# Optimization experiments

Measured on AMD Instinct MI355X. Metric: run time of the kernel, lower is better.

Reference implementation:

```python
import jax, jax.numpy as jnp
import numpy as np

N_FEATURES = 128
N_QUBITS = 10
Q_DEPTH = 4
N_OUTPUTS = 1
BATCH = 32768


def _apply_1q(psi, U, w, n):
    """Apply a single-qubit gate on wire w. psi: [B, 2^n]; U: [2,2] or [B,2,2]."""
    B = psi.shape[0]
    left, right = 2 ** w, 2 ** (n - 1 - w)
    psi = psi.reshape(B, left, 2, right)
    if U.ndim == 2:
        psi = jnp.einsum('ij,bljr->blir', U, psi)
    else:
        psi = jnp.einsum('bij,bljr->blir', U, psi)
    return psi.reshape(B, -1)


def _apply_cnot(psi, c, t, n):
    """CNOT(control=c, target=t) on psi [B, 2^n] (wire 0 = most significant bit)."""
    B = psi.shape[0]
    psi = psi.reshape((B,) + (2,) * n)
    ax_c, ax_t = c + 1, t + 1
    psi0 = jnp.take(psi, 0, axis=ax_c)
    psi1 = jnp.take(psi, 1, axis=ax_c)
    ax_t2 = ax_t - 1 if ax_t > ax_c else ax_t  # target axis shifts after removing control axis
    psi1 = jnp.flip(psi1, axis=ax_t2)          # flip target bit where control == 1
    psi = jnp.stack([psi0, psi1], axis=ax_c)
    return psi.reshape(B, -1)


def _rx_batched(theta):
    """RX(theta) per sample. theta: [B] -> U: [B,2,2] complex64."""
    c = jnp.cos(0.5 * theta).astype(jnp.complex64)
    s = jnp.sin(0.5 * theta).astype(jnp.complex64)
    row0 = jnp.stack([c, -1j * s], axis=-1)
    row1 = jnp.stack([-1j * s, c], axis=-1)
    return jnp.stack([row0, row1], axis=-2)


def _rot(phi, theta, omega):
    """Pennylane Rot = RZ(omega) @ RY(theta) @ RZ(phi), scalar angles -> [2,2] complex64."""
    c = jnp.cos(0.5 * theta)
    s = jnp.sin(0.5 * theta)
    u00 = jnp.exp(-0.5j * (phi + omega)) * c
    u01 = -jnp.exp(0.5j * (phi - omega)) * s
    u10 = jnp.exp(-0.5j * (phi - omega)) * s
    u11 = jnp.exp(0.5j * (phi + omega)) * c
    return jnp.stack([jnp.stack([u00, u01]), jnp.stack([u10, u11])]).astype(jnp.complex64)


def _quantum_forward(angles, q_weights):
    """Batched statevector sim: AngleEmbedding(RX) + StronglyEntanglingLayers, PauliZ expvals."""
    B, n = angles.shape
    depth = q_weights.shape[0]
    D = 2 ** n
    psi = jnp.zeros((B, D), jnp.complex64).at[:, 0].set(1.0)
    # AngleEmbedding: RX(angles[:, w]) on each wire (per-sample angles)
    for w in range(n):
        psi = _apply_1q(psi, _rx_batched(angles[:, w]), w, n)
    # StronglyEntanglingLayers: Rot on each wire, then CNOT ring with range r
    for l in range(depth):
        for w in range(n):
            U = _rot(q_weights[l, w, 0], q_weights[l, w, 1], q_weights[l, w, 2])
            psi = _apply_1q(psi, U, w, n)
        r = (l % (n - 1)) + 1
        for w in range(n):
            psi = _apply_cnot(psi, w, (w + r) % n, n)
    probs = psi.real ** 2 + psi.imag ** 2  # [B, D]
    # <Z_i> = sum_k probs[:,k] * (+1 if bit_i(k)==0 else -1); wire 0 = MSB
    bits = (jnp.arange(D)[None, :] >> (n - 1 - jnp.arange(n))[:, None]) & 1  # [n, D]
    signs = (1.0 - 2.0 * bits).astype(jnp.float32)
    return probs @ signs.T  # [B, n]


def setup_inputs() -> dict:
    key = jax.random.key(0)
    ks = jax.random.split(key, 5)
    x = jax.random.normal(ks[0], (BATCH, N_FEATURES), jnp.float32)
    W_pre = jax.random.normal(ks[1], (N_QUBITS, N_FEATURES), jnp.float32) / np.sqrt(N_FEATURES).astype(np.float32)
    b_pre = jnp.zeros((N_QUBITS,), jnp.float32)
    q_weights = 0.01 * jax.random.normal(ks[2], (Q_DEPTH, N_QUBITS, 3), jnp.float32)
    W_post = jax.random.normal(ks[3], (N_OUTPUTS, N_QUBITS), jnp.float32) / np.sqrt(N_QUBITS).astype(np.float32)
    b_post = jnp.zeros((N_OUTPUTS,), jnp.float32)
    return {"x": x, "W_pre": W_pre, "b_pre": b_pre, "q_weights": q_weights, "W_post": W_post, "b_post": b_post}


def reference(x, W_pre, b_pre, q_weights, W_post, b_post):
    angles = jnp.tanh(x @ W_pre.T + b_pre)        # pre_net + tanh -> [B, n_qubits]
    q_out = _quantum_forward(angles, q_weights)   # PauliZ expectations [B, n_qubits]
    return jax.nn.sigmoid(q_out @ W_post.T + b_post)
```

## Files before the change

kernel.cpp:

```cpp
#include <hip/hip_runtime.h>
#include <math.h>

#define BATCH 32768

typedef unsigned int u32;

#if defined(__has_builtin)
#if __has_builtin(__builtin_amdgcn_permlane32_swap) && __has_builtin(__builtin_amdgcn_permlane16_swap)
#define USE_PERMLANE 1
#else
#define USE_PERMLANE 0
#endif
#else
#define USE_PERMLANE 0
#endif

struct GateC { unsigned prt, sel; };
struct CircuitT { GateC g[4][10]; unsigned srow[10]; };

constexpr CircuitT make_circuit() {
  CircuitT C{};
  unsigned row[10], col[10];
  for (int b = 0; b < 10; ++b) { row[b] = 1u << b; col[b] = 1u << b; }
  for (int l = 0; l < 4; ++l) {
    for (int w = 0; w < 10; ++w) {
      C.g[l][w].prt = col[9 - w];
      C.g[l][w].sel = row[9 - w];
    }
    const int r = (l % 9) + 1;
    for (int w = 0; w < 10; ++w) {
      const int c = w, t = (w + r) % 10;
      const int bc = 9 - c, bt = 9 - t;
      row[bt] ^= row[bc];
      col[bc] ^= col[bt];
    }
  }
  for (int i = 0; i < 10; ++i) C.srow[i] = row[9 - i];
  return C;
}
constexpr CircuitT CIRC = make_circuit();

template<int CTRL>
__device__ __forceinline__ u32 dppu(u32 v) {
  return (u32)__builtin_amdgcn_update_dpp((int)v, (int)v, CTRL, 0xF, 0xF, false);
}

template<int LOW>
__device__ __forceinline__ u32 dpp_low(u32 v) {
  static_assert(LOW >= 0 && LOW <= 15, "bad mask");
  if constexpr (LOW == 0) return v;
  else if constexpr (LOW == 1) return dppu<0xB1>(v);
  else if constexpr (LOW == 2) return dppu<0x4E>(v);
  else if constexpr (LOW == 3) return dppu<0x1B>(v);
  else if constexpr (LOW == 7) return dppu<0x141>(v);
  else if constexpr (LOW == 15) return dppu<0x140>(v);
  else if constexpr (LOW >= 4 && LOW <= 6) return dpp_low<LOW ^ 7>(dppu<0x141>(v));
  else return dpp_low<LOW ^ 15>(dppu<0x140>(v));
}

constexpr int dpp_ops_low(int low) {
  if (low == 0) return 0;
  if (low == 1 || low == 2 || low == 3 || low == 7 || low == 15) return 1;
  if ((low >= 4 && low <= 6) || low == 8 || (low >= 12 && low <= 14)) return 2;
  return 3;
}
constexpr int chain_cost(int M) {
#if !USE_PERMLANE
  if (M & 48) return 99;
#endif
  return ((M & 32) ? 2 : 0) + ((M & 16) ? 2 : 0) + dpp_ops_low(M & 15);
}
constexpr bool use_ds_mask(int M) { return chain_cost(M) >= 2; }

#if USE_PERMLANE
__device__ __forceinline__ u32 xor16u(u32 v, int lane) {
  auto r = __builtin_amdgcn_permlane16_swap(v, v, false, false);
  return (lane & 16) ? r[0] : r[1];
}
__device__ __forceinline__ u32 xor32u(u32 v, int lane) {
  auto r = __builtin_amdgcn_permlane32_swap(v, v, false, false);
  return (lane & 32) ? r[0] : r[1];
}
#else
__device__ __forceinline__ u32 xor16u(u32 v, int lane) { return (u32)__shfl_xor((int)v, 16, 64); }
__device__ __forceinline__ u32 xor32u(u32 v, int lane) { return (u32)__shfl_xor((int)v, 32, 64); }
#endif

template<int M>
__device__ __forceinline__ u32 lshuf(u32 v, int lane, int bpa) {
  if constexpr (use_ds_mask(M)) {
    if constexpr ((M & 32) != 0) {
      return (u32)__builtin_amdgcn_ds_bpermute(bpa, (int)v);
    } else {
      return (u32)__builtin_amdgcn_ds_swizzle((int)v, 0x1F | (M << 10));
    }
  } else {
    u32 t = v;
    if constexpr ((M & 32) != 0) t = xor32u(t, lane);
    if constexpr ((M & 16) != 0) t = xor16u(t, lane);
    if constexpr ((M & 15) != 0) t = dpp_low<M & 15>(t);
    return t;
  }
}

template<int CTRL>
__device__ __forceinline__ float dppf(float v) {
  const int i = __float_as_int(v);
  return __int_as_float(__builtin_amdgcn_update_dpp(i, i, CTRL, 0xF, 0xF, false));
}
__device__ __forceinline__ float shflx(float v, int m) { return __shfl_xor(v, m, 64); }

__device__ __forceinline__ float wave_sum(float v, int lane) {
  v += dppf<0xB1>(v);
  v += dppf<0x4E>(v);
  v += dppf<0x141>(v);
  v += dppf<0x140>(v);
#if USE_PERMLANE
  { auto r = __builtin_amdgcn_permlane16_swap(__float_as_uint(v), __float_as_uint(v), false, false);
    v = __uint_as_float(r[0]) + __uint_as_float(r[1]); }
  { auto r = __builtin_amdgcn_permlane32_swap(__float_as_uint(v), __float_as_uint(v), false, false);
    v = __uint_as_float(r[0]) + __uint_as_float(r[1]); }
#else
  v += shflx(v, 16);
  v += shflx(v, 32);
#endif
  return v;
}

__device__ __forceinline__ u32 pk_mul_h(u32 a, u32 b) {
  u32 d; asm("v_pk_mul_f16 %0, %1, %2" : "=v"(d) : "v"(a), "v"(b)); return d;
}
__device__ __forceinline__ u32 pk_fma_h(u32 a, u32 b, u32 c) {
  u32 d; asm("v_pk_fma_f16 %0, %1, %2, %3" : "=v"(d) : "v"(a), "v"(b), "v"(c)); return d;
}
__device__ __forceinline__ u32 pk_fma_hsw(u32 a, u32 b, u32 c) {
  u32 d;
  asm("v_pk_fma_f16 %0, %1, %2, %3 op_sel:[1,0,0] op_sel_hi:[0,1,1]"
      : "=v"(d) : "v"(a), "v"(b), "v"(c));
  return d;
}

__device__ __forceinline__ u32 pk2(float lo, float hi) {
  auto h = __builtin_amdgcn_cvt_pkrtz(lo, hi);
  return __builtin_bit_cast(u32, h);
}

__device__ __forceinline__ u32 updh(u32 a, u32 q, const uint4 s) {
  u32 t = pk_mul_h(a, s.x);
  t = pk_fma_hsw(a, s.y, t);
  t = pk_fma_h(q, s.z, t);
  t = pk_fma_hsw(q, s.w, t);
  return t;
}

template<int L, int W>
__device__ __forceinline__ void gate(u32 a[16], const u32* __restrict__ Ush, int lane) {
  constexpr unsigned PRT = CIRC.g[L][W].prt;
  constexpr unsigned SEL = CIRC.g[L][W].sel;
  constexpr int PLm = (int)(PRT >> 4), PRm = (int)(PRT & 15u);
  constexpr int SLm = (int)(SEL >> 4), SRm = (int)(SEL & 15u);

  int hl = 0;
  if constexpr (SLm != 0) hl = __popc(lane & SLm) & 1;

  const u32* gb = Ush + (L * 10 + W - 10) * 8;
  const uint4 cA = *(const uint4*)(gb + (hl << 2));
  uint4 cB;
  if constexpr (SRm != 0) cB = *(const uint4*)(gb + ((hl ^ 1) << 2));
  else                    cB = cA;

  int bpa = 0;
  if constexpr (use_ds_mask(PLm) && (PLm & 32) != 0) bpa = (lane ^ PLm) << 2;

  if constexpr (PLm == 0) {
    constexpr int LB = PRm & (-PRm);
#pragma unroll
    for (int t0 = 0; t0 < 16; ++t0) {
      if (t0 & LB) continue;
      const int t1 = t0 ^ PRm;
      const uint4 s0 = (__builtin_popcount((unsigned)(t0 & SRm)) & 1) ? cB : cA;
      const uint4 s1 = (__builtin_popcount((unsigned)(t1 & SRm)) & 1) ? cB : cA;
      const u32 a0 = a[t0], a1 = a[t1];
      a[t0] = updh(a0, a1, s0);
      a[t1] = updh(a1, a0, s1);
    }
  } else if constexpr (PRm == 0) {
#pragma unroll
    for (int t = 0; t < 16; ++t) {
      const u32 q = lshuf<PLm>(a[t], lane, bpa);
      const uint4 s = (__builtin_popcount((unsigned)(t & SRm)) & 1) ? cB : cA;
      a[t] = updh(a[t], q, s);
    }
  } else {
    constexpr int LB = PRm & (-PRm);
#pragma unroll
    for (int t0 = 0; t0 < 16; ++t0) {
      if (t0 & LB) continue;
      const int t1 = t0 ^ PRm;
      const u32 q0 = lshuf<PLm>(a[t1], lane, bpa);
      const u32 q1 = lshuf<PLm>(a[t0], lane, bpa);
      const uint4 s0 = (__builtin_popcount((unsigned)(t0 & SRm)) & 1) ? cB : cA;
      const uint4 s1 = (__builtin_popcount((unsigned)(t1 & SRm)) & 1) ? cB : cA;
      a[t0] = updh(a[t0], q0, s0);
      a[t1] = updh(a[t1], q1, s1);
    }
  }
}

template<int L, int W>
__device__ __forceinline__ void layer_from(u32 a[16], const u32* __restrict__ Ush, int lane) {
  if constexpr (W < 10) {
    gate<L, W>(a, Ush, lane);
    layer_from<L, W + 1>(a, Ush, lane);
  }
}

__global__ __launch_bounds__(256, 4) void qnn_kernel(
    const float* __restrict__ x, const float* __restrict__ Wpre,
    const float* __restrict__ bpre, const float* __restrict__ qw,
    const float* __restrict__ Wpost, const float* __restrict__ bpost,
    float* __restrict__ out)
{
  __shared__ __align__(16) u32 Ush[320];

  const int tid = threadIdx.x;
  if (tid < 40) {
    const float phi = qw[tid * 3 + 0];
    const float th  = qw[tid * 3 + 1];
    const float om  = qw[tid * 3 + 2];
    const float c = cosf(0.5f * th), s_ = sinf(0.5f * th);
    const float A  = c;
    const float Br = -cosf(phi) * s_, Bi = -sinf(phi) * s_;
    const float Cr =  cosf(om)  * s_, Ci =  sinf(om)  * s_;
    const float Dr =  cosf(phi + om) * c, Di = sinf(phi + om) * c;
    if (tid < 10) {
      u32* q = &Ush[240 + tid * 8];
      q[0] = __float_as_uint(A);  q[1] = __float_as_uint(Br);
      q[2] = __float_as_uint(Bi); q[3] = __float_as_uint(Cr);
      q[4] = __float_as_uint(Ci); q[5] = __float_as_uint(Dr);
      q[6] = __float_as_uint(Di); q[7] = 0u;
    } else {
      u32* p = &Ush[(tid - 10) * 8];
      p[0] = pk2(A, A);   p[1] = pk2(0.f, 0.f);
      p[2] = pk2(Br, Br); p[3] = pk2(-Bi, Bi);
      p[4] = pk2(Dr, Dr); p[5] = pk2(-Di, Di);
      p[6] = pk2(Cr, Cr); p[7] = pk2(-Ci, Ci);
    }
  }
  __syncthreads();

  const int lane = tid & 63;
  const int b = blockIdx.x * 4 + (tid >> 6);

  const float* xrow = x + (size_t)b * 128;
  const float x0 = xrow[lane];
  const float x1 = xrow[lane + 64];
  float cw[10], sw[10];
#pragma unroll
  for (int w = 0; w < 10; ++w) {
    float p = fmaf(x0, Wpre[w * 128 + lane], x1 * Wpre[w * 128 + 64 + lane]);
    p = wave_sum(p, lane);
    const float e = __expf(2.f * (p + bpre[w]));
    const float ang = 1.f - 2.f * __builtin_amdgcn_rcpf(e + 1.f);
    const float h = 0.5f * ang;
    cw[w] = __cosf(h);
    sw[w] = __sinf(h);
  }

  float u0r[10], u0i[10], u1r[10], u1i[10];
#pragma unroll
  for (int w = 0; w < 10; ++w) {
    const u32* q = &Ush[240 + w * 8];
    const float A = __uint_as_float(q[0]), Br = __uint_as_float(q[1]);
    const float Bi = __uint_as_float(q[2]), Cr = __uint_as_float(q[3]);
    const float Ci = __uint_as_float(q[4]), Dr = __uint_as_float(q[5]);
    const float Di = __uint_as_float(q[6]);
    const float ch = cw[w], sh = sw[w];
    u0r[w] = fmaf(A, ch, Bi * sh);
    u0i[w] = -Br * sh;
    u1r[w] = fmaf(Cr, ch, Di * sh);
    u1i[w] = fmaf(Ci, ch, -Dr * sh);
  }

  float Lr, Li;
  {
    const int b0 = (lane >> 5) & 1;
    Lr = b0 ? u1r[0] : u0r[0];
    Li = b0 ? u1i[0] : u0i[0];
  }
#pragma unroll
  for (int w = 1; w < 6; ++w) {
    const int bb = (lane >> (5 - w)) & 1;
    const float arv = bb ? u1r[w] : u0r[w];
    const float aiv = bb ? u1i[w] : u0i[w];
    const float nr = fmaf(Lr, arv, -Li * aiv);
    const float ni = fmaf(Lr, aiv, Li * arv);
    Lr = nr; Li = ni;
  }

  float t4r[4], t4i[4], lsr[4], lsi[4];
#pragma unroll
  for (int aa = 0; aa < 2; ++aa) {
#pragma unroll
    for (int c2 = 0; c2 < 2; ++c2) {
      const int k = (aa << 1) | c2;
      const float ar6 = aa ? u1r[6] : u0r[6], ai6 = aa ? u1i[6] : u0i[6];
      const float ar7 = c2 ? u1r[7] : u0r[7], ai7 = c2 ? u1i[7] : u0i[7];
      t4r[k] = fmaf(ar6, ar7, -ai6 * ai7);
      t4i[k] = fmaf(ar6, ai7, ai6 * ar7);
      const float ar8 = aa ? u1r[8] : u0r[8], ai8 = aa ? u1i[8] : u0i[8];
      const float ar9 = c2 ? u1r[9] : u0r[9], ai9 = c2 ? u1i[9] : u0i[9];
      const float s4r = fmaf(ar8, ar9, -ai8 * ai9);
      const float s4i = fmaf(ar8, ai9, ai8 * ar9);
      lsr[k] = fmaf(s4r, Lr, -s4i * Li);
      lsi[k] = fmaf(s4r, Li, s4i * Lr);
    }
  }

  u32 a[16];
#pragma unroll
  for (int t = 0; t < 16; ++t) {
    const int hi4 = t >> 2, lo4 = t & 3;
    const float re = fmaf(t4r[hi4], lsr[lo4], -t4i[hi4] * lsi[lo4]);
    const float im = fmaf(t4r[hi4], lsi[lo4],  t4i[hi4] * lsr[lo4]);
    a[t] = pk2(re, im);
  }

  layer_from<1, 0>(a, Ush, lane);
  layer_from<2, 0>(a, Ush, lane);
  layer_from<3, 0>(a, Ush, lane);

  float Wl[10];
#pragma unroll
  for (int i = 0; i < 10; ++i) {
    const int sl = (int)(CIRC.srow[i] >> 4);
    const int par = __popc(lane & sl) & 1;
    const float wv = Wpost[i];
    Wl[i] = par ? -wv : wv;
  }
  float G[16];
#pragma unroll
  for (int m = 0; m < 16; ++m) G[m] = 0.f;
#pragma unroll
  for (int i = 0; i < 10; ++i) G[CIRC.srow[i] & 15u] += Wl[i];
#pragma unroll
  for (int bit = 1; bit < 16; bit <<= 1) {
#pragma unroll
    for (int m = 0; m < 16; ++m) {
      if (!(m & bit)) {
        const float t = G[m];
        G[m] = t + G[m ^ bit];
        G[m ^ bit] = t - G[m ^ bit];
      }
    }
  }

  union H2U { u32 u; _Float16 h[2]; };
  float acc = 0.f;
#pragma unroll
  for (int t = 0; t < 16; ++t) {
    H2U z; z.u = a[t];
    const float rr = (float)z.h[0];
    const float ii = (float)z.h[1];
    acc = fmaf(fmaf(rr, rr, ii * ii), G[t], acc);
  }
  acc = wave_sum(acc, lane);

  if (lane == 0) {
    const float z = acc + bpost[0];
    out[b] = __builtin_amdgcn_rcpf(1.f + __expf(-z));
  }
}

extern "C" void kernel_launch(void* const* d_in, const int* in_sizes, int n_in,
                              void* d_out, int out_size, void* d_ws, size_t ws_size,
                              hipStream_t stream) {
  const float* x     = (const float*)d_in[0];
  const float* Wpre  = (const float*)d_in[1];
  const float* bpre  = (const float*)d_in[2];
  const float* qw    = (const float*)d_in[3];
  const float* Wpost = (const float*)d_in[4];
  const float* bpost = (const float*)d_in[5];
  float* out = (float*)d_out;

  (void)in_sizes; (void)n_in; (void)out_size; (void)d_ws; (void)ws_size;

  qnn_kernel<<<BATCH / 4, 256, 0, stream>>>(x, Wpre, bpre, qw, Wpost, bpost, out);
}
```

Baseline: 170.4 us.

## Precompute post-readout weight table in LDS, reorder gates, use fdot2 for probabilities

Moves the per-lane Walsh-Hadamard computation of the readout weights G into a shared 16x64 table that each block fills once. Each wave then reads its weights from LDS instead of recomputing them. Gate application order within layers 1-3 is permuted, presumably to group commuting gates and cut shuffle cost. |a|^2 is computed with a packed fp16 fdot2. The table adds LDS use and per-block setup work, and the reorder relies on those gates commuting.

Result: no change. 167.5 us (-1.7%).

```diff
diff --git a/kernel.cpp b/kernel.cpp
--- a/kernel.cpp
+++ b/kernel.cpp
@@ -11,8 +11,14 @@
 #else
 #define USE_PERMLANE 0
 #endif
+#if __has_builtin(__builtin_amdgcn_fdot2)
+#define HAS_FDOT2 1
+#else
+#define HAS_FDOT2 0
+#endif
 #else
 #define USE_PERMLANE 0
+#define HAS_FDOT2 0
 #endif
 
 struct GateC { unsigned prt, sel; };
@@ -39,6 +45,13 @@
   return C;
 }
 constexpr CircuitT CIRC = make_circuit();
+
+constexpr int ORD[4][10] = {
+  {0,1,2,3,4,5,6,7,8,9},
+  {0,6,1,7,2,8,3,4,9,5},
+  {0,2,1,3,7,4,8,5,9,6},
+  {0,3,1,2,4,5,6,7,8,9},
+};
 
 template<int CTRL>
 __device__ __forceinline__ u32 dppu(u32 v) {
@@ -207,11 +220,11 @@
   }
 }
 
-template<int L, int W>
+template<int L, int K>
 __device__ __forceinline__ void layer_from(u32 a[16], const u32* __restrict__ Ush, int lane) {
-  if constexpr (W < 10) {
-    gate<L, W>(a, Ush, lane);
-    layer_from<L, W + 1>(a, Ush, lane);
+  if constexpr (K < 10) {
+    gate<L, ORD[L][K]>(a, Ush, lane);
+    layer_from<L, K + 1>(a, Ush, lane);
   }
 }
 
@@ -222,6 +235,7 @@
     float* __restrict__ out)
 {
   __shared__ __align__(16) u32 Ush[320];
+  __shared__ float gtab[16 * 64];
 
   const int tid = threadIdx.x;
   if (tid < 40) {
@@ -247,6 +261,22 @@
       p[6] = pk2(Cr, Cr); p[7] = pk2(-Ci, Ci);
     }
   }
+#pragma unroll
+  for (int k = 0; k < 4; ++k) {
+    const int idx = tid * 4 + k;
+    const int t = idx >> 6;
+    const int l6 = idx & 63;
+    float g = 0.f;
+#pragma unroll
+    for (int i = 0; i < 10; ++i) {
+      const int sl = (int)(CIRC.srow[i] >> 4);
+      const int sr = (int)(CIRC.srow[i] & 15u);
+      const int par = (__popc(l6 & sl) + __popc(t & sr)) & 1;
+      const float wv = Wpost[i];
+      g += par ? -wv : wv;
+    }
+    gtab[t * 64 + l6] = g;
+  }
   __syncthreads();
 
   const int lane = tid & 63;
@@ -330,39 +360,23 @@
   layer_from<2, 0>(a, Ush, lane);
   layer_from<3, 0>(a, Ush, lane);
 
-  float Wl[10];
-#pragma unroll
-  for (int i = 0; i < 10; ++i) {
-    const int sl = (int)(CIRC.srow[i] >> 4);
-    const int par = __popc(lane & sl) & 1;
-    const float wv = Wpost[i];
-    Wl[i] = par ? -wv : wv;
-  }
-  float G[16];
-#pragma unroll
-  for (int m = 0; m < 16; ++m) G[m] = 0.f;
-#pragma unroll
-  for (int i = 0; i < 10; ++i) G[CIRC.srow[i] & 15u] += Wl[i];
-#pragma unroll
-  for (int bit = 1; bit < 16; bit <<= 1) {
-#pragma unroll
-    for (int m = 0; m < 16; ++m) {
-      if (!(m & bit)) {
-        const float t = G[m];
-        G[m] = t + G[m ^ bit];
-        G[m ^ bit] = t - G[m ^ bit];
-      }
-    }
-  }
-
-  union H2U { u32 u; _Float16 h[2]; };
   float acc = 0.f;
 #pragma unroll
   for (int t = 0; t < 16; ++t) {
-    H2U z; z.u = a[t];
+    const float g = gtab[t * 64 + lane];
+    float p;
+#if HAS_FDOT2
+    typedef _Float16 h2 __attribute__((ext_vector_type(2)));
+    const h2 ah = __builtin_bit_cast(h2, a[t]);
+    p = __builtin_amdgcn_fdot2(ah, ah, 0.f, false);
+#else
+    union H2U { u32 u; _Float16 h[2]; } z;
+    z.u = a[t];
     const float rr = (float)z.h[0];
     const float ii = (float)z.h[1];
-    acc = fmaf(fmaf(rr, rr, ii * ii), G[t], acc);
+    p = fmaf(rr, rr, ii * ii);
+#endif
+    acc = fmaf(p, g, acc);
   }
   acc = wave_sum(acc, lane);
 
```
